# Optimization experiments

Measured on AMD Instinct MI355X. Metric: run time of the kernel, lower is better.

The kernel has to match this reference:

```python
import jax, jax.numpy as jnp
import numpy as np
from itertools import combinations_with_replacement

B, T, F, L, POLY_ORDER = 16, 2048, 128, 16, 3


def _hilbert_filter(N):
    # Matches pytorch_hilbert: H[0]=0, H[1:N//2]=2, H[N//2]=0 (even N)
    h = np.zeros(N, dtype=np.float32)
    if N % 2 == 0:
        h[1:N // 2] = 2.0
    else:
        h[1:(N + 1) // 2] = 2.0
    return jnp.asarray(h)


def hilbert(sig, axis=1):
    N = sig.shape[axis]
    Xf = jnp.fft.fft(sig, axis=axis)
    shape = [1] * sig.ndim
    shape[axis] = N
    return jnp.fft.ifft(Xf * _hilbert_filter(N).reshape(shape), axis=axis)


def _combo_indices(latent, poly_order):
    # static index arrays, grouped by degree n
    return [np.array(list(combinations_with_replacement(range(latent), n)), dtype=np.int32)
            for n in range(1, poly_order + 1)]


def compute_library(z, poly_order):
    # z: [B, T, L] -> theta: [B, T, library_dim]
    feats = []
    for combos in _combo_indices(z.shape[-1], poly_order):
        zc = z[..., combos]            # [B, T, ncomb, n]
        feats.append(jnp.prod(zc, axis=-1))  # [B, T, ncomb]
    analytic = hilbert(z, axis=1)
    feats.append(z)
    feats.append(jnp.abs(analytic))    # extract_real_component
    feats.append(jnp.angle(analytic))  # extract_imaginary_component
    return jnp.concatenate(feats, axis=-1)


def setup_inputs() -> dict:
    key = jax.random.key(0)
    ks = jax.random.split(key, 7)
    lib_dim = L + 2 * L + sum(len(c) for c in _combo_indices(L, POLY_ORDER))
    s_enc = 1.0 / np.sqrt(F)
    s_dec = 1.0 / np.sqrt(L)
    s_sin = 1.0 / np.sqrt(lib_dim)
    return {
        "x": jax.random.normal(ks[0], (B, T, F), dtype=jnp.float32),
        "W_enc": jax.random.uniform(ks[1], (L, F), jnp.float32, -s_enc, s_enc),
        "b_enc": jax.random.uniform(ks[2], (L,), jnp.float32, -s_enc, s_enc),
        "W_dec": jax.random.uniform(ks[3], (F, L), jnp.float32, -s_dec, s_dec),
        "b_dec": jax.random.uniform(ks[4], (F,), jnp.float32, -s_dec, s_dec),
        "W_sindy": jax.random.uniform(ks[5], (L, lib_dim), jnp.float32, -s_sin, s_sin),
        "b_sindy": jax.random.uniform(ks[6], (L,), jnp.float32, -s_sin, s_sin),
    }


def reference(x, W_enc, b_enc, W_dec, b_dec, W_sindy, b_sindy):
    z = jnp.einsum('btf,lf->btl', x, W_enc) + b_enc          # encoder
    theta = compute_library(z, POLY_ORDER)                    # [B,T,lib_dim]
    y_hat = jnp.einsum('btd,ld->btl', theta, W_sindy) + b_sindy
    x_hat = jnp.einsum('btl,fl->btf', z, W_dec) + b_dec       # decoder
    # Jacobian of the linear encoder w.r.t. x is the constant weight matrix
    # broadcast per (b, t): identical math to the O((B*T)^2) autograd version.
    jac_z_x = jnp.broadcast_to(W_enc, (x.shape[0], x.shape[1], L, F))
    return (y_hat, x_hat, z, jac_z_x, W_sindy, W_dec)
```

## Files before the change

### kernel.cpp

```cpp
#include <hip/hip_runtime.h>
#include <math.h>

typedef unsigned short u16;
typedef unsigned int   u32;
typedef __attribute__((ext_vector_type(4))) float f32x4;

#define OFF_ZWS   0
#define OFF_AT    524288
#define OFF_PT    1048576
#define OFF_WT    1572864
#define OFF_ZT    1589120
#define OFF_TWC   2113408
#define OFF_TWS   2115456
#define OFF_PART  2117504

#define HEAD_F4   1577952
#define R1_LO     1577952
#define R1_HI     6577952
#define R2_LO     6577952
#define R2_HI     11577952
#define R3_LO     11577952
#define R3_HI     16777216

__device__ __forceinline__ void jac_range(const float* __restrict__ Wenc,
                                          float* __restrict__ out_jac,
                                          int lo, int hi, int idx, int nth)
{
    const float* wsrc = Wenc + (size_t)((lo + idx) & 511) * 4;
    f32x4 w;
    w.x = wsrc[0]; w.y = wsrc[1]; w.z = wsrc[2]; w.w = wsrc[3];
    f32x4* j4 = (f32x4*)out_jac;
    for (int i = lo + idx; i < hi; i += nth)
        __builtin_nontemporal_store(w, j4 + i);
}

__global__ __launch_bounds__(256) void k1_encdec(
    const float* __restrict__ x, const float* __restrict__ Wenc, const float* __restrict__ benc,
    const float* __restrict__ Wdec, const float* __restrict__ bdec,
    const float* __restrict__ Wsin,
    float* __restrict__ out_z, float* __restrict__ out_xhat,
    float* __restrict__ out_Ws, float* __restrict__ out_Wd,
    float* __restrict__ z_ws, float* __restrict__ z_t, float* __restrict__ wt,
    double* __restrict__ twc_g, double* __restrict__ tws_g,
    float* __restrict__ out_jac)
{
    int tid = threadIdx.x;
    int blk = blockIdx.x;

    if (blk >= 2116) {
        jac_range(Wenc, out_jac, R1_LO, R1_HI, (blk - 2116) * 256 + tid, 262144);
        return;
    }
    if (blk >= 2048) {
        int t0 = (blk - 2048) * 256 + tid;
        if (t0 < 16256) {
            float v = Wsin[t0];
            out_Ws[t0] = v;
            int l = t0 / 1016;
            int d = t0 - l * 1016;
            if (d < 16) v += Wsin[t0 + 968];
            wt[d * 16 + l] = v;
        } else if (t0 < 17280) {
            int k = t0 - 16256;
            double ang = -6.283185307179586476925286766559 * (double)k / 2048.0;
            double s_, c_;
            sincos(ang, &s_, &c_);
            twc_g[k] = c_;
            tws_g[k] = s_;
        }
        if (t0 < 2048) out_Wd[t0] = Wdec[t0];
        return;
    }

    __shared__ float xs[16][128];
    __shared__ float we[16][132];
    __shared__ float wd[128][17];
    __shared__ float zs[16][16];

    {
        const float4* xv = (const float4*)x + (size_t)blk * 512;
        float* dst = &xs[0][0];
        float4 a = xv[tid], b = xv[tid + 256];
        dst[tid*4+0]=a.x; dst[tid*4+1]=a.y; dst[tid*4+2]=a.z; dst[tid*4+3]=a.w;
        dst[(tid+256)*4+0]=b.x; dst[(tid+256)*4+1]=b.y; dst[(tid+256)*4+2]=b.z; dst[(tid+256)*4+3]=b.w;
    }
    {
        const float4* wev = (const float4*)Wenc;
        #pragma unroll
        for (int h = 0; h < 2; ++h) {
            int vi = tid + h * 256;
            float4 v = wev[vi];
            int base = vi * 4, row = base >> 7, col = base & 127;
            we[row][col+0]=v.x; we[row][col+1]=v.y; we[row][col+2]=v.z; we[row][col+3]=v.w;
        }
    }
    {
        const float4* wdv = (const float4*)Wdec;
        #pragma unroll
        for (int h = 0; h < 2; ++h) {
            int vi = tid + h * 256;
            float4 v = wdv[vi];
            int base = vi * 4, row = base >> 4, col = base & 15;
            wd[row][col+0]=v.x; wd[row][col+1]=v.y; wd[row][col+2]=v.z; wd[row][col+3]=v.w;
        }
    }
    __syncthreads();

    {
        int r = tid >> 4, l = tid & 15;
        float s = 0.f;
        #pragma unroll 8
        for (int f = 0; f < 128; ++f) s += xs[r][f] * we[l][f];
        float zv = s + benc[l];
        zs[r][l] = zv;
        int zo = blk * 256 + tid;
        z_ws[zo]  = zv;
        out_z[zo] = zv;
    }
    __syncthreads();

    {
        int l2 = tid >> 4, r2 = tid & 15;
        z_t[l2 * 32768 + blk * 16 + r2] = zs[r2][l2];
    }

    #pragma unroll
    for (int u = 0; u < 8; ++u) {
        int idx = u * 256 + tid;
        int rr = idx >> 7, f = idx & 127;
        float acc = bdec[f];
        #pragma unroll
        for (int ll = 0; ll < 16; ++ll) acc += zs[rr][ll] * wd[f][ll];
        out_xhat[(size_t)blk * 2048 + idx] = acc;
    }
}

__global__ __launch_bounds__(1024) void k2_hilbert(
    const float* __restrict__ z_t, const double* __restrict__ twc_g,
    const double* __restrict__ tws_g, const float* __restrict__ Wenc,
    float* __restrict__ a_t, float* __restrict__ p_t,
    float* __restrict__ out_jac)
{
    __shared__ double2 c[2048];
    __shared__ double2 tw[1024];

    int tid = threadIdx.x;
    if (blockIdx.x >= 256) {
        jac_range(Wenc, out_jac, R2_LO, R2_HI, (blockIdx.x - 256) * 1024 + tid, 524288);
        return;
    }
    int b = blockIdx.x >> 4, l = blockIdx.x & 15;
    const size_t base = (size_t)l * 32768 + (size_t)b * 2048;
    const float* zp = z_t + base;

    {
        double2 t; t.x = twc_g[tid]; t.y = tws_g[tid];
        tw[tid] = t;
    }
    {
        double2 v0; v0.x = (double)zp[tid];        v0.y = 0.0;
        double2 v1; v1.x = (double)zp[tid + 1024]; v1.y = 0.0;
        c[tid] = v0;
        c[tid + 1024] = v1;
    }
    __syncthreads();

    for (int half = 1024; half >= 1; half >>= 1) {
        int step = 1024 / half;
        int j = tid & (half - 1);
        int pos = ((tid - j) << 1) + j;
        double2 u = c[pos], v = c[pos + half];
        double2 w = tw[j * step];
        double2 s, dsc;
        s.x = u.x + v.x;  s.y = u.y + v.y;
        double br = u.x - v.x, bi = u.y - v.y;
        dsc.x = br * w.x - bi * w.y;
        dsc.y = br * w.y + bi * w.x;
        c[pos] = s;
        c[pos + half] = dsc;
        __syncthreads();
    }

    #pragma unroll
    for (int h = 0; h < 2; ++h) {
        int t = tid + h * 1024;
        double sc = (t == 0 || (t & 1)) ? 0.0 : (2.0 / 2048.0);
        double2 v = c[t];
        v.x *= sc; v.y *= sc;
        c[t] = v;
    }
    __syncthreads();

    for (int half = 1; half <= 1024; half <<= 1) {
        int step = 1024 / half;
        int j = tid & (half - 1);
        int pos = ((tid - j) << 1) + j;
        double2 u = c[pos], v = c[pos + half];
        double2 w = tw[j * step];
        double tr = v.x * w.x + v.y * w.y;
        double ti = v.y * w.x - v.x * w.y;
        double2 p0, p1;
        p0.x = u.x + tr; p0.y = u.y + ti;
        p1.x = u.x - tr; p1.y = u.y - ti;
        c[pos] = p0;
        c[pos + half] = p1;
        __syncthreads();
    }

    #pragma unroll
    for (int h = 0; h < 2; ++h) {
        int t = tid + h * 1024;
        double2 v = c[t];
        a_t[base + t] = (float)sqrt(v.x * v.x + v.y * v.y);
        p_t[base + t] = (float)atan2(v.y, v.x);
    }
}

#define EMIT2(EXPR) do {                                                    \
    if ((unsigned)(d - LO) < 121u) {                                        \
        float vv[2];                                                        \
        _Pragma("unroll") for (int p = 0; p < 2; ++p) vv[p] = (EXPR);       \
        int bb = (d - LO) << 4;                                             \
        _Pragma("unroll") for (int l = 0; l < 16; ++l) {                    \
            float w = lw[bb + l];                                           \
            acc[0][l] = fmaf(vv[0], w, acc[0][l]);                          \
            acc[1][l] = fmaf(vv[1], w, acc[1][l]);                          \
        }                                                                   \
    }                                                                       \
    ++d;                                                                    \
} while (0)

__global__ __launch_bounds__(256, 2) void k3_yhat(
    const float* __restrict__ z_ws, const float* __restrict__ wt,
    const float* __restrict__ Wenc,
    float* __restrict__ part, float* __restrict__ out_jac)
{
    __shared__ float lw[1936];
    int tid = threadIdx.x;
    if (blockIdx.x >= 512) {
        jac_range(Wenc, out_jac, R3_LO, R3_HI, (blockIdx.x - 512) * 256 + tid, 262144);
        return;
    }
    int slice = blockIdx.x >> 6;
    int ptgrp = blockIdx.x & 63;
    int LO = slice * 121;
    int base = ptgrp * 512;

    {
        const float4* src = (const float4*)(wt + LO * 16);
        float4* dst = (float4*)lw;
        for (int i = tid; i < 484; i += 256) dst[i] = src[i];
    }
    __syncthreads();

    float z[2][16], acc[2][16];
    #pragma unroll
    for (int p = 0; p < 2; ++p) {
        int bt = base + p * 256 + tid;
        const float4* zp = (const float4*)(z_ws + (size_t)bt * 16);
        #pragma unroll
        for (int q = 0; q < 4; ++q) {
            float4 v = zp[q];
            z[p][q*4+0]=v.x; z[p][q*4+1]=v.y; z[p][q*4+2]=v.z; z[p][q*4+3]=v.w;
        }
    }
    #pragma unroll
    for (int p = 0; p < 2; ++p)
        #pragma unroll
        for (int l = 0; l < 16; ++l) acc[p][l] = 0.f;

    int d = 0;
    #pragma unroll
    for (int i = 0; i < 16; ++i) EMIT2(z[p][i]);
    #pragma unroll
    for (int i = 0; i < 16; ++i)
        #pragma unroll
        for (int j = i; j < 16; ++j) EMIT2(z[p][i] * z[p][j]);
    #pragma unroll
    for (int i = 0; i < 16; ++i)
        #pragma unroll
        for (int j = i; j < 16; ++j)
            #pragma unroll
            for (int k = j; k < 16; ++k) EMIT2(z[p][i] * z[p][j] * z[p][k]);

    #pragma unroll
    for (int p = 0; p < 2; ++p) {
        int bt = base + p * 256 + tid;
        float4* pp = (float4*)(part + (size_t)slice * 524288 + (size_t)bt * 16);
        #pragma unroll
        for (int q = 0; q < 4; ++q) {
            float4 v;
            v.x = acc[p][q*4+0]; v.y = acc[p][q*4+1];
            v.z = acc[p][q*4+2]; v.w = acc[p][q*4+3];
            pp[q] = v;
        }
    }
}

__global__ __launch_bounds__(256) void k3_tail(
    const float* __restrict__ part, const float* __restrict__ a_t,
    const float* __restrict__ p_t, const float* __restrict__ wt,
    const float* __restrict__ bsin, float* __restrict__ out_y)
{
    __shared__ float lw[512];
    int tid = threadIdx.x;
    if (tid < 128) {
        ((float4*)lw)[tid] = ((const float4*)(wt + 984 * 16))[tid];
    }
    __syncthreads();

    int bt = blockIdx.x * 256 + tid;
    float acc[16];
    {
        const float4* bp = (const float4*)bsin;
        #pragma unroll
        for (int q = 0; q < 4; ++q) {
            float4 v = bp[q];
            acc[q*4+0]=v.x; acc[q*4+1]=v.y; acc[q*4+2]=v.z; acc[q*4+3]=v.w;
        }
    }
    #pragma unroll
    for (int sl = 0; sl < 8; ++sl) {
        const float4* pp = (const float4*)(part + (size_t)sl * 524288 + (size_t)bt * 16);
        #pragma unroll
        for (int q = 0; q < 4; ++q) {
            float4 v = pp[q];
            acc[q*4+0]+=v.x; acc[q*4+1]+=v.y; acc[q*4+2]+=v.z; acc[q*4+3]+=v.w;
        }
    }
    #pragma unroll
    for (int i = 0; i < 16; ++i) {
        float av = a_t[(size_t)i * 32768 + bt];
        #pragma unroll
        for (int l = 0; l < 16; ++l) acc[l] = fmaf(av, lw[i * 16 + l], acc[l]);
    }
    #pragma unroll
    for (int i = 0; i < 16; ++i) {
        float pv = p_t[(size_t)i * 32768 + bt];
        #pragma unroll
        for (int l = 0; l < 16; ++l) acc[l] = fmaf(pv, lw[256 + i * 16 + l], acc[l]);
    }

    float4* yp = (float4*)(out_y + (size_t)bt * 16);
    #pragma unroll
    for (int q = 0; q < 4; ++q) {
        float4 v;
        v.x = acc[q*4+0]; v.y = acc[q*4+1]; v.z = acc[q*4+2]; v.w = acc[q*4+3];
        yp[q] = v;
    }
}

__global__ __launch_bounds__(256) void k4_jac_head(
    const float* __restrict__ Wenc, float* __restrict__ out_jac)
{
    jac_range(Wenc, out_jac, 0, HEAD_F4, blockIdx.x * 256 + threadIdx.x, 393216);
}

extern "C" void kernel_launch(void* const* d_in, const int* in_sizes, int n_in,
                              void* d_out, int out_size, void* d_ws, size_t ws_size,
                              hipStream_t stream)
{
    const float* x  = (const float*)d_in[0];
    const float* We = (const float*)d_in[1];
    const float* be = (const float*)d_in[2];
    const float* Wd = (const float*)d_in[3];
    const float* bd = (const float*)d_in[4];
    const float* Ws = (const float*)d_in[5];
    const float* bs = (const float*)d_in[6];

    float* out  = (float*)d_out;
    float* o_y  = out;
    float* o_xh = out + 524288;
    float* o_z  = out + 4718592;
    float* o_j  = out + 5242880;
    float* o_Ws = out + 72351744;
    float* o_Wd = out + 72368000;

    float*  z_ws  = o_j + OFF_ZWS;
    float*  a_t   = o_j + OFF_AT;
    float*  p_t   = o_j + OFF_PT;
    float*  wt    = o_j + OFF_WT;
    float*  z_t   = o_j + OFF_ZT;
    double* twc_g = (double*)(o_j + OFF_TWC);
    double* tws_g = (double*)(o_j + OFF_TWS);
    float*  part  = o_j + OFF_PART;

    hipLaunchKernelGGL(k1_encdec, dim3(3140), dim3(256), 0, stream,
                       x, We, be, Wd, bd, Ws, o_z, o_xh, o_Ws, o_Wd,
                       z_ws, z_t, wt, twc_g, tws_g, o_j);
    hipLaunchKernelGGL(k2_hilbert, dim3(768), dim3(1024), 0, stream,
                       z_t, twc_g, tws_g, We, a_t, p_t, o_j);
    hipLaunchKernelGGL(k3_yhat, dim3(1536), dim3(256), 0, stream,
                       z_ws, wt, We, part, o_j);
    hipLaunchKernelGGL(k3_tail, dim3(128), dim3(256), 0, stream,
                       part, a_t, p_t, wt, bs, o_y);
    hipLaunchKernelGGL(k4_jac_head, dim3(1536), dim3(256), 0, stream,
                       We, o_j);
}
```

Before: 380.5 us.

## Fuse y_hat slices and tail into one kernel with in-block LDS reduction

Moves the scratch buffers from the Jacobian output region into the workspace, which lets the Jacobian broadcast be split into three equal ranges spread over the three kernels and removes the separate head kernel. The y_hat kernel now uses 512-thread blocks where each wave handles one 128-term slice of the library, and the Hilbert amplitude/phase terms are folded into the wave that covers them. The eight partial sums are combined by a tree reduction in LDS instead of being written to a global partial buffer and summed in a tail kernel. In exchange it needs a large LDS allocation (about 64 KB for the whole weight table), which may lower occupancy, and adds several block-wide barriers.

```diff
diff --git a/kernel.cpp b/kernel.cpp
--- a/kernel.cpp
+++ b/kernel.cpp
@@ -5,22 +5,19 @@
 typedef unsigned int   u32;
 typedef __attribute__((ext_vector_type(4))) float f32x4;
 
-#define OFF_ZWS   0
-#define OFF_AT    524288
-#define OFF_PT    1048576
-#define OFF_WT    1572864
-#define OFF_ZT    1589120
-#define OFF_TWC   2113408
-#define OFF_TWS   2115456
-#define OFF_PART  2117504
-
-#define HEAD_F4   1577952
-#define R1_LO     1577952
-#define R1_HI     6577952
-#define R2_LO     6577952
-#define R2_HI     11577952
-#define R3_LO     11577952
-#define R3_HI     16777216
+#define OFF_AT    0
+#define OFF_PT    524288
+#define OFF_WT    1048576
+#define OFF_ZT    1064832
+#define OFF_TWC   1589120
+#define OFF_TWS   1591168
+
+#define R1_LO 0
+#define R1_HI 5592576
+#define R2_LO 5592576
+#define R2_HI 11185152
+#define R3_LO 11185152
+#define R3_HI 16777216
 
 __device__ __forceinline__ void jac_range(const float* __restrict__ Wenc,
                                           float* __restrict__ out_jac,
@@ -40,7 +37,7 @@
     const float* __restrict__ Wsin,
     float* __restrict__ out_z, float* __restrict__ out_xhat,
     float* __restrict__ out_Ws, float* __restrict__ out_Wd,
-    float* __restrict__ z_ws, float* __restrict__ z_t, float* __restrict__ wt,
+    float* __restrict__ z_t, float* __restrict__ wt,
     double* __restrict__ twc_g, double* __restrict__ tws_g,
     float* __restrict__ out_jac)
 {
@@ -113,9 +110,7 @@
         for (int f = 0; f < 128; ++f) s += xs[r][f] * we[l][f];
         float zv = s + benc[l];
         zs[r][l] = zv;
-        int zo = blk * 256 + tid;
-        z_ws[zo]  = zv;
-        out_z[zo] = zv;
+        out_z[blk * 256 + tid] = zv;
     }
     __syncthreads();
 
@@ -217,47 +212,49 @@
 }
 
 #define EMIT2(EXPR) do {                                                    \
-    if ((unsigned)(d - LO) < 121u) {                                        \
-        float vv[2];                                                        \
-        _Pragma("unroll") for (int p = 0; p < 2; ++p) vv[p] = (EXPR);       \
-        int bb = (d - LO) << 4;                                             \
+    if ((unsigned)(d - LO) < 128u) {                                        \
+        float v0, v1;                                                       \
+        { const int p = 0; v0 = (EXPR); }                                   \
+        { const int p = 1; v1 = (EXPR); }                                   \
+        int bb = d << 4;             \
         _Pragma("unroll") for (int l = 0; l < 16; ++l) {                    \
-            float w = lw[bb + l];                                           \
-            acc[0][l] = fmaf(vv[0], w, acc[0][l]);                          \
-            acc[1][l] = fmaf(vv[1], w, acc[1][l]);                          \
+            float w = lds[bb + l];                                          \
+            acc[0][l] = fmaf(v0, w, acc[0][l]);                             \
+            acc[1][l] = fmaf(v1, w, acc[1][l]);                             \
         }                                                                   \
     }                                                                       \
     ++d;                                                                    \
 } while (0)
 
-__global__ __launch_bounds__(256, 2) void k3_yhat(
-    const float* __restrict__ z_ws, const float* __restrict__ wt,
-    const float* __restrict__ Wenc,
-    float* __restrict__ part, float* __restrict__ out_jac)
+__global__ __launch_bounds__(512) void k3_yhat(
+    const float* __restrict__ z_g, const float* __restrict__ a_t,
+    const float* __restrict__ p_t, const float* __restrict__ wt,
+    const float* __restrict__ bsin, const float* __restrict__ Wenc,
+    float* __restrict__ out_y, float* __restrict__ out_jac)
 {
-    __shared__ float lw[1936];
+    __shared__ float lds[16256];
     int tid = threadIdx.x;
-    if (blockIdx.x >= 512) {
-        jac_range(Wenc, out_jac, R3_LO, R3_HI, (blockIdx.x - 512) * 256 + tid, 262144);
+    if (blockIdx.x >= 256) {
+        jac_range(Wenc, out_jac, R3_LO, R3_HI, (blockIdx.x - 256) * 512 + tid, 524288);
         return;
     }
-    int slice = blockIdx.x >> 6;
-    int ptgrp = blockIdx.x & 63;
-    int LO = slice * 121;
-    int base = ptgrp * 512;
-
-    {
-        const float4* src = (const float4*)(wt + LO * 16);
-        float4* dst = (float4*)lw;
-        for (int i = tid; i < 484; i += 256) dst[i] = src[i];
+    int wave = tid >> 6;
+    int lane = tid & 63;
+    int LO = wave << 7;
+    int B0 = blockIdx.x << 7;
+
+    {
+        const float4* src = (const float4*)wt;
+        float4* dst = (float4*)lds;
+        for (int i = tid; i < 4064; i += 512) dst[i] = src[i];
     }
     __syncthreads();
 
     float z[2][16], acc[2][16];
     #pragma unroll
     for (int p = 0; p < 2; ++p) {
-        int bt = base + p * 256 + tid;
-        const float4* zp = (const float4*)(z_ws + (size_t)bt * 16);
+        int bt = B0 + (lane << 1) + p;
+        const float4* zp = (const float4*)(z_g + (size_t)bt * 16);
         #pragma unroll
         for (int q = 0; q < 4; ++q) {
             float4 v = zp[q];
@@ -282,78 +279,106 @@
         for (int j = i; j < 16; ++j)
             #pragma unroll
             for (int k = j; k < 16; ++k) EMIT2(z[p][i] * z[p][j] * z[p][k]);
-
-    #pragma unroll
-    for (int p = 0; p < 2; ++p) {
-        int bt = base + p * 256 + tid;
-        float4* pp = (float4*)(part + (size_t)slice * 524288 + (size_t)bt * 16);
-        #pragma unroll
-        for (int q = 0; q < 4; ++q) {
+    if ((unsigned)(984 - LO) < 128u) {
+        #pragma unroll
+        for (int i = 0; i < 16; ++i) {
+            int bb = (984 + i) << 4;
+            float a0 = a_t[(size_t)i * 32768 + B0 + (lane << 1)];
+            float a1 = a_t[(size_t)i * 32768 + B0 + (lane << 1) + 1];
+            #pragma unroll
+            for (int l = 0; l < 16; ++l) {
+                float w = lds[bb + l];
+                acc[0][l] = fmaf(a0, w, acc[0][l]);
+                acc[1][l] = fmaf(a1, w, acc[1][l]);
+            }
+        }
+        #pragma unroll
+        for (int i = 0; i < 16; ++i) {
+            int bb = (1000 + i) << 4;
+            float p0 = p_t[(size_t)i * 32768 + B0 + (lane << 1)];
+            float p1 = p_t[(size_t)i * 32768 + B0 + (lane << 1) + 1];
+            #pragma unroll
+            for (int l = 0; l < 16; ++l) {
+                float w = lds[bb + l];
+                acc[0][l] = fmaf(p0, w, acc[0][l]);
+                acc[1][l] = fmaf(p1, w, acc[1][l]);
+            }
+        }
+    }
+
+    __syncthreads();
+    if (wave >= 4) {
+        int w = wave - 4;
+        #pragma unroll
+        for (int p = 0; p < 2; ++p) {
+            float* dst = lds + w * 2048 + ((lane << 1) + p) * 16;
+            #pragma unroll
+            for (int l = 0; l < 16; ++l) dst[l] = acc[p][l];
+        }
+    }
+    __syncthreads();
+    if (wave < 4) {
+        #pragma unroll
+        for (int p = 0; p < 2; ++p) {
+            const float* src = lds + wave * 2048 + ((lane << 1) + p) * 16;
+            #pragma unroll
+            for (int l = 0; l < 16; ++l) acc[p][l] += src[l];
+        }
+    }
+    __syncthreads();
+    if (wave == 2 || wave == 3) {
+        int w = wave - 2;
+        #pragma unroll
+        for (int p = 0; p < 2; ++p) {
+            float* dst = lds + w * 2048 + ((lane << 1) + p) * 16;
+            #pragma unroll
+            for (int l = 0; l < 16; ++l) dst[l] = acc[p][l];
+        }
+    }
+    __syncthreads();
+    if (wave < 2) {
+        #pragma unroll
+        for (int p = 0; p < 2; ++p) {
+            const float* src = lds + wave * 2048 + ((lane << 1) + p) * 16;
+            #pragma unroll
+            for (int l = 0; l < 16; ++l) acc[p][l] += src[l];
+        }
+    }
+    __syncthreads();
+    if (wave == 1) {
+        #pragma unroll
+        for (int p = 0; p < 2; ++p) {
+            float* dst = lds + ((lane << 1) + p) * 16;
+            #pragma unroll
+            for (int l = 0; l < 16; ++l) dst[l] = acc[p][l];
+        }
+    }
+    __syncthreads();
+    if (wave == 0) {
+        const float4* bp = (const float4*)bsin;
+        float4 b0 = bp[0], b1 = bp[1], b2 = bp[2], b3 = bp[3];
+        #pragma unroll
+        for (int p = 0; p < 2; ++p) {
+            const float* src = lds + ((lane << 1) + p) * 16;
+            #pragma unroll
+            for (int l = 0; l < 16; ++l) acc[p][l] += src[l];
+            int bt = B0 + (lane << 1) + p;
+            float4* yp = (float4*)(out_y + (size_t)bt * 16);
             float4 v;
-            v.x = acc[p][q*4+0]; v.y = acc[p][q*4+1];
-            v.z = acc[p][q*4+2]; v.w = acc[p][q*4+3];
-            pp[q] = v;
-        }
-    }
-}
-
-__global__ __launch_bounds__(256) void k3_tail(
-    const float* __restrict__ part, const float* __restrict__ a_t,
-    const float* __restrict__ p_t, const float* __restrict__ wt,
-    const float* __restrict__ bsin, float* __restrict__ out_y)
-{
-    __shared__ float lw[512];
-    int tid = threadIdx.x;
-    if (tid < 128) {
-        ((float4*)lw)[tid] = ((const float4*)(wt + 984 * 16))[tid];
-    }
-    __syncthreads();
-
-    int bt = blockIdx.x * 256 + tid;
-    float acc[16];
-    {
-        const float4* bp = (const float4*)bsin;
-        #pragma unroll
-        for (int q = 0; q < 4; ++q) {
-            float4 v = bp[q];
-            acc[q*4+0]=v.x; acc[q*4+1]=v.y; acc[q*4+2]=v.z; acc[q*4+3]=v.w;
-        }
-    }
-    #pragma unroll
-    for (int sl = 0; sl < 8; ++sl) {
-        const float4* pp = (const float4*)(part + (size_t)sl * 524288 + (size_t)bt * 16);
-        #pragma unroll
-        for (int q = 0; q < 4; ++q) {
-            float4 v = pp[q];
-            acc[q*4+0]+=v.x; acc[q*4+1]+=v.y; acc[q*4+2]+=v.z; acc[q*4+3]+=v.w;
-        }
-    }
-    #pragma unroll
-    for (int i = 0; i < 16; ++i) {
-        float av = a_t[(size_t)i * 32768 + bt];
-        #pragma unroll
-        for (int l = 0; l < 16; ++l) acc[l] = fmaf(av, lw[i * 16 + l], acc[l]);
-    }
-    #pragma unroll
-    for (int i = 0; i < 16; ++i) {
-        float pv = p_t[(size_t)i * 32768 + bt];
-        #pragma unroll
-        for (int l = 0; l < 16; ++l) acc[l] = fmaf(pv, lw[256 + i * 16 + l], acc[l]);
-    }
-
-    float4* yp = (float4*)(out_y + (size_t)bt * 16);
-    #pragma unroll
-    for (int q = 0; q < 4; ++q) {
-        float4 v;
-        v.x = acc[q*4+0]; v.y = acc[q*4+1]; v.z = acc[q*4+2]; v.w = acc[q*4+3];
-        yp[q] = v;
-    }
-}
-
-__global__ __launch_bounds__(256) void k4_jac_head(
-    const float* __restrict__ Wenc, float* __restrict__ out_jac)
-{
-    jac_range(Wenc, out_jac, 0, HEAD_F4, blockIdx.x * 256 + threadIdx.x, 393216);
+            v.x = acc[p][0] + b0.x;  v.y = acc[p][1] + b0.y;
+            v.z = acc[p][2] + b0.z;  v.w = acc[p][3] + b0.w;
+            yp[0] = v;
+            v.x = acc[p][4] + b1.x;  v.y = acc[p][5] + b1.y;
+            v.z = acc[p][6] + b1.z;  v.w = acc[p][7] + b1.w;
+            yp[1] = v;
+            v.x = acc[p][8] + b2.x;  v.y = acc[p][9] + b2.y;
+            v.z = acc[p][10] + b2.z; v.w = acc[p][11] + b2.w;
+            yp[2] = v;
+            v.x = acc[p][12] + b3.x; v.y = acc[p][13] + b3.y;
+            v.z = acc[p][14] + b3.z; v.w = acc[p][15] + b3.w;
+            yp[3] = v;
+        }
+    }
 }
 
 extern "C" void kernel_launch(void* const* d_in, const int* in_sizes, int n_in,
@@ -376,24 +401,19 @@
     float* o_Ws = out + 72351744;
     float* o_Wd = out + 72368000;
 
-    float*  z_ws  = o_j + OFF_ZWS;
-    float*  a_t   = o_j + OFF_AT;
-    float*  p_t   = o_j + OFF_PT;
-    float*  wt    = o_j + OFF_WT;
-    float*  z_t   = o_j + OFF_ZT;
-    double* twc_g = (double*)(o_j + OFF_TWC);
-    double* tws_g = (double*)(o_j + OFF_TWS);
-    float*  part  = o_j + OFF_PART;
+    float*  ws    = (float*)d_ws;
+    float*  a_t   = ws + OFF_AT;
+    float*  p_t   = ws + OFF_PT;
+    float*  wt    = ws + OFF_WT;
+    float*  z_t   = ws + OFF_ZT;
+    double* twc_g = (double*)(ws + OFF_TWC);
+    double* tws_g = (double*)(ws + OFF_TWS);
 
     hipLaunchKernelGGL(k1_encdec, dim3(3140), dim3(256), 0, stream,
                        x, We, be, Wd, bd, Ws, o_z, o_xh, o_Ws, o_Wd,
-                       z_ws, z_t, wt, twc_g, tws_g, o_j);
+                       z_t, wt, twc_g, tws_g, o_j);
     hipLaunchKernelGGL(k2_hilbert, dim3(768), dim3(1024), 0, stream,
                        z_t, twc_g, tws_g, We, a_t, p_t, o_j);
-    hipLaunchKernelGGL(k3_yhat, dim3(1536), dim3(256), 0, stream,
-                       z_ws, wt, We, part, o_j);
-    hipLaunchKernelGGL(k3_tail, dim3(128), dim3(256), 0, stream,
-                       part, a_t, p_t, wt, bs, o_y);
-    hipLaunchKernelGGL(k4_jac_head, dim3(1536), dim3(256), 0, stream,
-                       We, o_j);
+    hipLaunchKernelGGL(k3_yhat, dim3(1280), dim3(512), 0, stream,
+                       o_z, a_t, p_t, wt, bs, We, o_y, o_j);
 }
```

Result: slower. 397.9 us (+4.6%).

## Move scratch buffers to workspace, drop jac head kernel, pad Hilbert LDS

Applied to the files above, without the earlier changes.

Intermediate buffers (a_t, p_t, z_t, twiddles, partials) move from the head of the Jacobian output region into the separate workspace. This removes the final kernel that rewrote the Jacobian head, and the three Jacobian-fill ranges are rebalanced to cover the whole output. The separate z_ws copy is dropped in favour of reading out_z directly. The FFT shared memory gains padding, with split cos/sin twiddle arrays, to reduce LDS bank conflicts. The trade-off is one fewer launch and one fewer duplicate store, at the cost of extra index arithmetic in the FFT and a dependence on the workspace being large enough.

```diff
diff --git a/kernel.cpp b/kernel.cpp
--- a/kernel.cpp
+++ b/kernel.cpp
@@ -5,22 +5,19 @@
 typedef unsigned int   u32;
 typedef __attribute__((ext_vector_type(4))) float f32x4;
 
-#define OFF_ZWS   0
-#define OFF_AT    524288
-#define OFF_PT    1048576
-#define OFF_WT    1572864
-#define OFF_ZT    1589120
-#define OFF_TWC   2113408
-#define OFF_TWS   2115456
-#define OFF_PART  2117504
-
-#define HEAD_F4   1577952
-#define R1_LO     1577952
-#define R1_HI     6577952
-#define R2_LO     6577952
-#define R2_HI     11577952
-#define R3_LO     11577952
-#define R3_HI     16777216
+#define OFF_AT    0
+#define OFF_PT    524288
+#define OFF_WT    1048576
+#define OFF_ZT    1064832
+#define OFF_TWC   1589120
+#define OFF_TWS   1591168
+
+#define R1_LO 0
+#define R1_HI 5592576
+#define R2_LO 5592576
+#define R2_HI 11185152
+#define R3_LO 11185152
+#define R3_HI 16777216
 
 __device__ __forceinline__ void jac_range(const float* __restrict__ Wenc,
                                           float* __restrict__ out_jac,
@@ -40,7 +37,7 @@
     const float* __restrict__ Wsin,
     float* __restrict__ out_z, float* __restrict__ out_xhat,
     float* __restrict__ out_Ws, float* __restrict__ out_Wd,
-    float* __restrict__ z_ws, float* __restrict__ z_t, float* __restrict__ wt,
+    float* __restrict__ z_t, float* __restrict__ wt,
     double* __restrict__ twc_g, double* __restrict__ tws_g,
     float* __restrict__ out_jac)
 {
@@ -113,9 +110,7 @@
         for (int f = 0; f < 128; ++f) s += xs[r][f] * we[l][f];
         float zv = s + benc[l];
         zs[r][l] = zv;
-        int zo = blk * 256 + tid;
-        z_ws[zo]  = zv;
-        out_z[zo] = zv;
+        out_z[blk * 256 + tid] = zv;
     }
     __syncthreads();
 
@@ -134,6 +129,9 @@
         out_xhat[(size_t)blk * 2048 + idx] = acc;
     }
 }
+
+#define TWPAD(k) ((k) + ((k) >> 5))
+#define CP(i)    ((i) + ((i) >> 4))
 
 __global__ __launch_bounds__(1024) void k2_hilbert(
     const float* __restrict__ z_t, const double* __restrict__ twc_g,
@@ -141,8 +139,9 @@
     float* __restrict__ a_t, float* __restrict__ p_t,
     float* __restrict__ out_jac)
 {
-    __shared__ double2 c[2048];
-    __shared__ double2 tw[1024];
+    __shared__ double2 c[2176];
+    __shared__ double twc_s[1056];
+    __shared__ double tws_s[1056];
 
     int tid = threadIdx.x;
     if (blockIdx.x >= 256) {
@@ -154,14 +153,14 @@
     const float* zp = z_t + base;
 
     {
-        double2 t; t.x = twc_g[tid]; t.y = tws_g[tid];
-        tw[tid] = t;
+        twc_s[TWPAD(tid)] = twc_g[tid];
+        tws_s[TWPAD(tid)] = tws_g[tid];
     }
     {
         double2 v0; v0.x = (double)zp[tid];        v0.y = 0.0;
         double2 v1; v1.x = (double)zp[tid + 1024]; v1.y = 0.0;
-        c[tid] = v0;
-        c[tid + 1024] = v1;
+        c[CP(tid)] = v0;
+        c[CP(tid + 1024)] = v1;
     }
     __syncthreads();
 
@@ -169,15 +168,17 @@
         int step = 1024 / half;
         int j = tid & (half - 1);
         int pos = ((tid - j) << 1) + j;
-        double2 u = c[pos], v = c[pos + half];
-        double2 w = tw[j * step];
+        int pa = CP(pos), pb = CP(pos + half);
+        int ti = TWPAD(j * step);
+        double2 u = c[pa], v = c[pb];
+        double wc = twc_s[ti], wsn = tws_s[ti];
         double2 s, dsc;
         s.x = u.x + v.x;  s.y = u.y + v.y;
         double br = u.x - v.x, bi = u.y - v.y;
-        dsc.x = br * w.x - bi * w.y;
-        dsc.y = br * w.y + bi * w.x;
-        c[pos] = s;
-        c[pos + half] = dsc;
+        dsc.x = br * wc - bi * wsn;
+        dsc.y = br * wsn + bi * wc;
+        c[pa] = s;
+        c[pb] = dsc;
         __syncthreads();
     }
 
@@ -185,9 +186,10 @@
     for (int h = 0; h < 2; ++h) {
         int t = tid + h * 1024;
         double sc = (t == 0 || (t & 1)) ? 0.0 : (2.0 / 2048.0);
-        double2 v = c[t];
+        int ci = CP(t);
+        double2 v = c[ci];
         v.x *= sc; v.y *= sc;
-        c[t] = v;
+        c[ci] = v;
     }
     __syncthreads();
 
@@ -195,22 +197,24 @@
         int step = 1024 / half;
         int j = tid & (half - 1);
         int pos = ((tid - j) << 1) + j;
-        double2 u = c[pos], v = c[pos + half];
-        double2 w = tw[j * step];
-        double tr = v.x * w.x + v.y * w.y;
-        double ti = v.y * w.x - v.x * w.y;
+        int pa = CP(pos), pb = CP(pos + half);
+        int ti = TWPAD(j * step);
+        double2 u = c[pa], v = c[pb];
+        double wc = twc_s[ti], wsn = tws_s[ti];
+        double tr = v.x * wc + v.y * wsn;
+        double ti2 = v.y * wc - v.x * wsn;
         double2 p0, p1;
-        p0.x = u.x + tr; p0.y = u.y + ti;
-        p1.x = u.x - tr; p1.y = u.y - ti;
-        c[pos] = p0;
-        c[pos + half] = p1;
+        p0.x = u.x + tr; p0.y = u.y + ti2;
+        p1.x = u.x - tr; p1.y = u.y - ti2;
+        c[pa] = p0;
+        c[pb] = p1;
         __syncthreads();
     }
 
     #pragma unroll
     for (int h = 0; h < 2; ++h) {
         int t = tid + h * 1024;
-        double2 v = c[t];
+        double2 v = c[CP(t)];
         a_t[base + t] = (float)sqrt(v.x * v.x + v.y * v.y);
         p_t[base + t] = (float)atan2(v.y, v.x);
     }
@@ -350,12 +354,6 @@
     }
 }
 
-__global__ __launch_bounds__(256) void k4_jac_head(
-    const float* __restrict__ Wenc, float* __restrict__ out_jac)
-{
-    jac_range(Wenc, out_jac, 0, HEAD_F4, blockIdx.x * 256 + threadIdx.x, 393216);
-}
-
 extern "C" void kernel_launch(void* const* d_in, const int* in_sizes, int n_in,
                               void* d_out, int out_size, void* d_ws, size_t ws_size,
                               hipStream_t stream)
@@ -376,24 +374,22 @@
     float* o_Ws = out + 72351744;
     float* o_Wd = out + 72368000;
 
-    float*  z_ws  = o_j + OFF_ZWS;
-    float*  a_t   = o_j + OFF_AT;
-    float*  p_t   = o_j + OFF_PT;
-    float*  wt    = o_j + OFF_WT;
-    float*  z_t   = o_j + OFF_ZT;
-    double* twc_g = (double*)(o_j + OFF_TWC);
-    double* tws_g = (double*)(o_j + OFF_TWS);
-    float*  part  = o_j + OFF_PART;
+    float*  ws    = (float*)d_ws;
+    float*  a_t   = ws + OFF_AT;
+    float*  p_t   = ws + OFF_PT;
+    float*  wt    = ws + OFF_WT;
+    float*  z_t   = ws + OFF_ZT;
+    double* twc_g = (double*)(ws + OFF_TWC);
+    double* tws_g = (double*)(ws + OFF_TWS);
+    float*  part  = ws + 1593216;
 
     hipLaunchKernelGGL(k1_encdec, dim3(3140), dim3(256), 0, stream,
                        x, We, be, Wd, bd, Ws, o_z, o_xh, o_Ws, o_Wd,
-                       z_ws, z_t, wt, twc_g, tws_g, o_j);
+                       z_t, wt, twc_g, tws_g, o_j);
     hipLaunchKernelGGL(k2_hilbert, dim3(768), dim3(1024), 0, stream,
                        z_t, twc_g, tws_g, We, a_t, p_t, o_j);
     hipLaunchKernelGGL(k3_yhat, dim3(1536), dim3(256), 0, stream,
-                       z_ws, wt, We, part, o_j);
+                       o_z, wt, We, part, o_j);
     hipLaunchKernelGGL(k3_tail, dim3(128), dim3(256), 0, stream,
                        part, a_t, p_t, wt, bs, o_y);
-    hipLaunchKernelGGL(k4_jac_head, dim3(1536), dim3(256), 0, stream,
-                       We, o_j);
-}
+}
```

Result: no change. 374.8 us, median of 2 (-1.5%).
